# Kernel tuning notes

Hardware: AMD Instinct MI355X
Metric: run time of the kernel (lower is better)

The kernel has to match this reference:

```python
import jax, jax.numpy as jnp
import numpy as np

B, T, C = 4, 2048, 1024
H = 16
DH = C // H  # 64


def setup_inputs() -> dict:
    key = jax.random.key(0)
    ks = jax.random.split(key, 6)
    s = 1.0 / np.sqrt(C)
    x = jax.random.normal(ks[0], (B, T, C), dtype=jnp.float32)
    # per-head projection weights, stacked: (H, C, DH)
    Wq = jax.random.uniform(ks[1], (H, C, DH), dtype=jnp.float32, minval=-s, maxval=s)
    Wk = jax.random.uniform(ks[2], (H, C, DH), dtype=jnp.float32, minval=-s, maxval=s)
    Wv = jax.random.uniform(ks[3], (H, C, DH), dtype=jnp.float32, minval=-s, maxval=s)
    # output projection (torch Linear: y = x @ W.T + b); store as (C, C) for x @ Wo
    Wo = jax.random.uniform(ks[4], (C, C), dtype=jnp.float32, minval=-s, maxval=s)
    bo = jax.random.uniform(ks[5], (C,), dtype=jnp.float32, minval=-s, maxval=s)
    return {"x": x, "Wq": Wq, "Wk": Wk, "Wv": Wv, "Wo": Wo, "bo": bo}


def reference(x, Wq, Wk, Wv, Wo, bo):
    # x: (B,T,C) -> q,k,v: (B,H,T,DH)
    q = jnp.einsum('btc,hcd->bhtd', x, Wq)
    k = jnp.einsum('btc,hcd->bhtd', x, Wk)
    v = jnp.einsum('btc,hcd->bhtd', x, Wv)
    scale = DH ** -0.5
    scores = jnp.einsum('bhtd,bhsd->bhts', q, k) * scale  # (B,H,T,T)
    causal = jnp.tril(jnp.ones((T, T), dtype=bool))
    scores = jnp.where(causal, scores, -jnp.inf)
    wei = jax.nn.softmax(scores, axis=-1)
    out = jnp.einsum('bhts,bhsd->bhtd', wei, v)  # (B,H,T,DH)
    # concat heads: (B,T,H*DH) = (B,T,C)
    out = out.transpose(0, 2, 1, 3).reshape(B, T, C)
    return out @ Wo + bo
```

## Files before the change

### kernel.cpp

```cpp
#include <hip/hip_runtime.h>

#define T_SEQ 2048
#define C_DIM 1024
#define H_NUM 16
#define DHD   64
#define B_NUM 4
#define M_ROWS (B_NUM*T_SEQ)

typedef __bf16 bf16x8 __attribute__((ext_vector_type(8)));
typedef float  f32x4  __attribute__((ext_vector_type(4)));
typedef unsigned short ushort8 __attribute__((ext_vector_type(8)));
typedef unsigned short ushort4e __attribute__((ext_vector_type(4)));

__device__ __forceinline__ unsigned short f2b(float f){
  return __builtin_bit_cast(unsigned short, (__bf16)f);
}
__device__ __forceinline__ bf16x8 as_bf(ushort8 u){ return __builtin_bit_cast(bf16x8, u); }
__device__ __forceinline__ float exp2fast(float x){ return __builtin_amdgcn_exp2f(x); }

__device__ __forceinline__ void gload16(const void* g, void* l){
  __builtin_amdgcn_global_load_lds(
      (const __attribute__((address_space(1))) void*)g,
      (__attribute__((address_space(3))) void*)l, 16, 0, 0);
}

#define MF(a,b,c) __builtin_amdgcn_mfma_f32_16x16x32_bf16(a,b,c,0,0,0)

__global__ __launch_bounds__(256) void k_prep(const float* __restrict__ x,
                                              const float* __restrict__ wq,
                                              const float* __restrict__ wk,
                                              const float* __restrict__ wv,
                                              const float* __restrict__ wo,
                                              unsigned short* __restrict__ xb,
                                              unsigned short* __restrict__ wt,
                                              unsigned short* __restrict__ wot){
  const int bid = blockIdx.x;
  if (bid < 8192){
    int i = bid*256 + threadIdx.x;
    float4 f = ((const float4*)x)[i];
    ushort4e o;
    o[0]=f2b(f.x); o[1]=f2b(f.y); o[2]=f2b(f.z); o[3]=f2b(f.w);
    ((ushort4e*)xb)[i] = o;
  } else {
    int idx = (bid - 8192)*256 + threadIdx.x;
    if (idx < 3*C_DIM*C_DIM){
      int nall = idx >> 10; int c = idx & 1023;
      int m = nall >> 10;   int n = nall & 1023;
      int h = n >> 6, d = n & 63;
      const float* w = (m==0) ? wq : (m==1) ? wk : wv;
      float f = w[((size_t)h*C_DIM + c)*DHD + d];
      if (m == 0) f *= 0.125f * 1.4426950408889634f;
      wt[idx] = f2b(f);
    } else {
      int j = idx - 3*C_DIM*C_DIM;
      int n = j >> 10, c = j & 1023;
      wot[j] = f2b(wo[(size_t)c*C_DIM + n]);
    }
  }
}

__global__ __launch_bounds__(256) void k_gemm_qkv(const unsigned short* __restrict__ xb,
                                                  const unsigned short* __restrict__ wt,
                                                  unsigned short* __restrict__ qo,
                                                  unsigned short* __restrict__ ko,
                                                  unsigned short* __restrict__ vtr){
  __shared__ __align__(16) unsigned short smem[2][128*64];
  const int tid = threadIdx.x, lane = tid & 63, wid = tid >> 6;
  const int g = lane >> 4, tl = lane & 15;
  const int wr = wid >> 1, wc = wid & 1;
  const int id = blockIdx.x;
  const int xcd = id & 7, i = id >> 3;
  const int xm = xcd >> 1, xn = xcd & 1;
  const int mbase = (xm*16 + i/12) * 128, nbase = (xn*12 + i%12) * 128;
  f32x4 acc[4][4] = {};
  for (int kk = 0; kk < C_DIM; kk += 64){
    __syncthreads();
    #pragma unroll
    for (int i2 = 0; i2 < 4; i2++){
      const int brow = (wid*4 + i2)*8;
      const int row  = brow + (lane >> 3);
      const int jj   = (lane & 7) ^ (row & 7);
      gload16(&xb[(size_t)(mbase+row)*C_DIM + kk + jj*8], &smem[0][brow*64]);
      gload16(&wt[(size_t)(nbase+row)*C_DIM + kk + jj*8], &smem[1][brow*64]);
    }
    __syncthreads();
    bf16x8 aF[4][2], bF[4][2];
    #pragma unroll
    for (int mb = 0; mb < 4; mb++){
      const int row = wr*64 + mb*16 + tl; const int s7 = row & 7;
      aF[mb][0] = as_bf(*(const ushort8*)&smem[0][row*64 + ((g     ^ s7)*8)]);
      aF[mb][1] = as_bf(*(const ushort8*)&smem[0][row*64 + (((4+g) ^ s7)*8)]);
    }
    #pragma unroll
    for (int nb = 0; nb < 4; nb++){
      const int row = wc*64 + nb*16 + tl; const int s7 = row & 7;
      bF[nb][0] = as_bf(*(const ushort8*)&smem[1][row*64 + ((g     ^ s7)*8)]);
      bF[nb][1] = as_bf(*(const ushort8*)&smem[1][row*64 + (((4+g) ^ s7)*8)]);
    }
    #pragma unroll
    for (int mb = 0; mb < 4; mb++)
      #pragma unroll
      for (int nb = 0; nb < 4; nb++){
        acc[mb][nb] = MF(aF[mb][0], bF[nb][0], acc[mb][nb]);
        acc[mb][nb] = MF(aF[mb][1], bF[nb][1], acc[mb][nb]);
      }
  }
  const int sel = nbase >> 10;
  if (sel < 2){
    unsigned short* dst0 = (sel == 0) ? qo : ko;
    #pragma unroll
    for (int mb = 0; mb < 4; mb++){
      #pragma unroll
      for (int nb = 0; nb < 4; nb++){
        #pragma unroll
        for (int r = 0; r < 4; r++){
          int gr = mbase + wr*64 + mb*16 + g*4 + r;
          int gc = nbase + wc*64 + nb*16 + tl;
          int b = gr >> 11, t = gr & 2047;
          int nw = gc & 1023;
          int h = nw >> 6, d = nw & 63;
          dst0[(((size_t)(b*H_NUM + h))*T_SEQ + t)*DHD + d] = f2b(acc[mb][nb][r]);
        }
      }
    }
  } else {
    __syncthreads();
    unsigned short* tr = &smem[0][0];
    #pragma unroll
    for (int mb = 0; mb < 4; mb++){
      #pragma unroll
      for (int nb = 0; nb < 4; nb++){
        const int n = wc*64 + nb*16 + tl;
        const int m0 = wr*64 + mb*16 + g*4;
        ushort4e pk;
        #pragma unroll
        for (int r = 0; r < 4; r++) pk[r] = f2b(acc[mb][nb][r]);
        *(ushort4e*)&tr[n*128 + (m0 ^ ((n & 15) << 3))] = pk;
      }
    }
    __syncthreads();
    const int hbase = (nbase - 2048) >> 6;
    const int b = mbase >> 11, tloc = mbase & 2047;
    const int n = tid >> 1, half = tid & 1;
    unsigned short* vdst = vtr + (((size_t)(b*H_NUM + hbase + (n >> 6)))*DHD + (n & 63))*T_SEQ
                           + tloc + half*64;
    const int nx = (n & 15) << 3;
    #pragma unroll
    for (int c8 = 0; c8 < 8; c8++){
      const int t0 = half*64 + (c8 >> 2)*32 + (c8 & 3)*4;
      ushort4e lo = *(const ushort4e*)&tr[n*128 + ((t0     ) ^ nx)];
      ushort4e hi = *(const ushort4e*)&tr[n*128 + ((t0 + 16) ^ nx)];
      ushort8 u;
      #pragma unroll
      for (int e = 0; e < 4; e++){ u[e] = lo[e]; u[4+e] = hi[e]; }
      *(ushort8*)&vdst[c8*8] = u;
    }
  }
}

__global__ __launch_bounds__(512) void k_flash(const unsigned short* __restrict__ q,
                                               const unsigned short* __restrict__ k,
                                               const unsigned short* __restrict__ vtg,
                                               unsigned short* __restrict__ o){
  __shared__ __align__(16) unsigned short kbufs[2][128*64];
  __shared__ __align__(16) unsigned short vbufs[2][64*128];
  const int tid = threadIdx.x, lane = tid & 63, w = tid >> 6;
  const int g = lane >> 4, tl = lane & 15;
  const int id = blockIdx.x;
  const int swz = (id & 7)*32 + (id >> 3);
  const int bh = swz >> 2, bx = swz & 3;
  const int b = bh >> 4, h = bh & 15;
  const unsigned short* qb = q   + (size_t)bh * T_SEQ * DHD;
  const unsigned short* kb = k   + (size_t)bh * T_SEQ * DHD;
  const unsigned short* vb = vtg + (size_t)bh * (size_t)DHD * T_SEQ;
  const int lrow = lane >> 3, lj = lane & 7;
  const int s7 = tl & 7;
  const int vre = lane >> 4;
  const int vh  = (lane >> 3) & 1;
  const int vcc = lane & 7;

  for (int pass = 0; pass < 2; ++pass){
    const int qt = pass ? (7 - bx) : bx;
    const int tbase = qt * 256;
    const int trow0 = tbase + w * 32;
    const int tmax = trow0 + 31;
    bf16x8 qF[2][2];
    #pragma unroll
    for (int tf = 0; tf < 2; tf++)
      #pragma unroll
      for (int ks = 0; ks < 2; ks++)
        qF[tf][ks] = as_bf(*(const ushort8*)&qb[(size_t)(trow0 + tf*16 + tl)*DHD + ks*32 + g*8]);
    f32x4 acc[2][4] = {};
    float mreg[2] = {-1e30f, -1e30f}, lreg[2] = {0.f, 0.f};
    const int nkt = 2*qt + 2;
    #pragma unroll
    for (int i = 0; i < 2; i++){
      const int krow = i*64 + w*8 + lrow;
      const int kjj  = lj ^ (krow & 7);
      gload16(&kb[(size_t)krow*DHD + kjj*8], &kbufs[0][(i*64 + w*8)*64]);
      const int vrow = i*32 + w*4 + vre;
      const int vjj  = vcc ^ (vrow & 7);
      gload16(&vb[(size_t)vrow*T_SEQ + vh*64 + vjj*8], &vbufs[0][(i*32 + w*4)*128]);
    }
    __syncthreads();
    for (int kti = 0; kti < nkt; ++kti){
      const int cur = kti & 1;
      const int kbase = kti * 128;
      if (kti + 1 < nkt){
        const int kb2 = kbase + 128;
        #pragma unroll
        for (int i = 0; i < 2; i++){
          const int krow = i*64 + w*8 + lrow;
          const int kjj  = lj ^ (krow & 7);
          gload16(&kb[(size_t)(kb2+krow)*DHD + kjj*8], &kbufs[cur^1][(i*64 + w*8)*64]);
          const int vrow = i*32 + w*4 + vre;
          const int vjj  = vcc ^ (vrow & 7);
          gload16(&vb[(size_t)vrow*T_SEQ + kb2 + vh*64 + vjj*8], &vbufs[cur^1][(i*32 + w*4)*128]);
        }
      }
      if (kbase <= tmax){
        const unsigned short* kcur = kbufs[cur];
        const unsigned short* vcur = vbufs[cur];
        f32x4 st[2][8] = {};
        __builtin_amdgcn_s_setprio(1);
        #pragma unroll
        for (int sf = 0; sf < 8; sf++){
          const int row = sf*16 + tl;
          const int r7 = row & 7;
          bf16x8 kf0 = as_bf(*(const ushort8*)&kcur[row*64 + ((g     ^ r7)*8)]);
          bf16x8 kf1 = as_bf(*(const ushort8*)&kcur[row*64 + (((4+g) ^ r7)*8)]);
          #pragma unroll
          for (int tf = 0; tf < 2; tf++){
            st[tf][sf] = MF(kf0, qF[tf][0], st[tf][sf]);
            st[tf][sf] = MF(kf1, qF[tf][1], st[tf][sf]);
          }
        }
        __builtin_amdgcn_s_setprio(0);
        if (kbase + 127 > trow0){
          #pragma unroll
          for (int tf = 0; tf < 2; tf++){
            int tg = trow0 + tf*16 + tl;
            #pragma unroll
            for (int sf = 0; sf < 8; sf++)
              #pragma unroll
              for (int r = 0; r < 4; r++)
                if (kbase + sf*16 + g*4 + r > tg) st[tf][sf][r] = -1e30f;
          }
        }
        bf16x8 pa[2][4];
        #pragma unroll
        for (int tf = 0; tf < 2; tf++){
          float mloc = -1e30f;
          #pragma unroll
          for (int sf = 0; sf < 8; sf++)
            #pragma unroll
            for (int r = 0; r < 4; r++) mloc = fmaxf(mloc, st[tf][sf][r]);
          if (__any(mloc > mreg[tf] + 8.f)){
            float mrow = fmaxf(mloc, __shfl_xor(mloc, 16));
            mrow = fmaxf(mrow, __shfl_xor(mrow, 32));
            float mnew = fmaxf(mreg[tf], mrow);
            float alpha = exp2fast(mreg[tf] - mnew);
            mreg[tf] = mnew;
            lreg[tf] *= alpha;
            #pragma unroll
            for (int df = 0; df < 4; df++)
              #pragma unroll
              for (int r = 0; r < 4; r++) acc[tf][df][r] *= alpha;
          }
          float sum = 0.f;
          #pragma unroll
          for (int q4 = 0; q4 < 4; q4++){
            ushort8 u;
            #pragma unroll
            for (int r = 0; r < 4; r++){
              float p0 = exp2fast(st[tf][2*q4  ][r] - mreg[tf]);
              float p1 = exp2fast(st[tf][2*q4+1][r] - mreg[tf]);
              sum += p0 + p1;
              u[r]   = f2b(p0);
              u[4+r] = f2b(p1);
            }
            pa[tf][q4] = as_bf(u);
          }
          lreg[tf] += sum;
        }
        __builtin_amdgcn_s_setprio(1);
        #pragma unroll
        for (int df = 0; df < 4; df++){
          const int row = df*16 + tl;
          bf16x8 vfr[4];
          #pragma unroll
          for (int q4 = 0; q4 < 4; q4++)
            vfr[q4] = as_bf(*(const ushort8*)&vcur[row*128 + (q4 >> 1)*64 + (((4*(q4 & 1) + g) ^ s7)*8)]);
          #pragma unroll
          for (int tf = 0; tf < 2; tf++)
            #pragma unroll
            for (int q4 = 0; q4 < 4; q4++)
              acc[tf][df] = MF(vfr[q4], pa[tf][q4], acc[tf][df]);
        }
        __builtin_amdgcn_s_setprio(0);
      }
      __syncthreads();
    }
    #pragma unroll
    for (int tf = 0; tf < 2; tf++){
      float l = lreg[tf];
      l += __shfl_xor(l, 16);
      l += __shfl_xor(l, 32);
      float inv = 1.f / l;
      int tg = trow0 + tf*16 + tl;
      #pragma unroll
      for (int df = 0; df < 4; df++){
        ushort4e ov;
        #pragma unroll
        for (int r = 0; r < 4; r++) ov[r] = f2b(acc[tf][df][r] * inv);
        *(ushort4e*)&o[((size_t)(b*T_SEQ + tg))*C_DIM + h*DHD + df*16 + g*4] = ov;
      }
    }
  }
}

__global__ __launch_bounds__(256) void k_gemm_proj(const unsigned short* __restrict__ ab,
                                                   const unsigned short* __restrict__ wot,
                                                   const float* __restrict__ bo,
                                                   float* __restrict__ out){
  __shared__ __align__(16) unsigned short a_lds[128*64];
  __shared__ __align__(16) unsigned short b_lds[128*64];
  const int tid = threadIdx.x, lane = tid & 63, wid = tid >> 6;
  const int g = lane >> 4, tl = lane & 15;
  const int wr = wid >> 1, wc = wid & 1;
  const int id = blockIdx.x;
  const int swz = (id & 7)*64 + (id >> 3);
  const int mbase = (swz >> 3) * 128, nbase = (swz & 7) * 128;
  f32x4 acc[4][4] = {};
  for (int kk = 0; kk < C_DIM; kk += 64){
    __syncthreads();
    #pragma unroll
    for (int i = 0; i < 4; i++){
      const int brow = (wid*4 + i)*8;
      const int row  = brow + (lane >> 3);
      const int jj   = (lane & 7) ^ (row & 7);
      gload16(&ab[(size_t)(mbase+row)*C_DIM + kk + jj*8],  &a_lds[brow*64]);
      gload16(&wot[(size_t)(nbase+row)*C_DIM + kk + jj*8], &b_lds[brow*64]);
    }
    __syncthreads();
    bf16x8 aF[4][2], bF[4][2];
    #pragma unroll
    for (int mb = 0; mb < 4; mb++){
      const int row = wr*64 + mb*16 + tl; const int s7 = row & 7;
      aF[mb][0] = as_bf(*(const ushort8*)&a_lds[row*64 + ((g     ^ s7)*8)]);
      aF[mb][1] = as_bf(*(const ushort8*)&a_lds[row*64 + (((4+g) ^ s7)*8)]);
    }
    #pragma unroll
    for (int nb = 0; nb < 4; nb++){
      const int row = wc*64 + nb*16 + tl; const int s7 = row & 7;
      bF[nb][0] = as_bf(*(const ushort8*)&b_lds[row*64 + ((g     ^ s7)*8)]);
      bF[nb][1] = as_bf(*(const ushort8*)&b_lds[row*64 + (((4+g) ^ s7)*8)]);
    }
    #pragma unroll
    for (int mb = 0; mb < 4; mb++)
      #pragma unroll
      for (int nb = 0; nb < 4; nb++){
        acc[mb][nb] = MF(aF[mb][0], bF[nb][0], acc[mb][nb]);
        acc[mb][nb] = MF(aF[mb][1], bF[nb][1], acc[mb][nb]);
      }
  }
  #pragma unroll
  for (int mb = 0; mb < 4; mb++){
    #pragma unroll
    for (int nb = 0; nb < 4; nb++){
      #pragma unroll
      for (int r = 0; r < 4; r++){
        int gr = mbase + wr*64 + mb*16 + g*4 + r;
        int gc = nbase + wc*64 + nb*16 + tl;
        out[(size_t)gr*C_DIM + gc] = acc[mb][nb][r] + bo[gc];
      }
    }
  }
}

extern "C" void kernel_launch(void* const* d_in, const int* in_sizes, int n_in,
                              void* d_out, int out_size, void* d_ws, size_t ws_size,
                              hipStream_t stream){
  const float* x  = (const float*)d_in[0];
  const float* Wq = (const float*)d_in[1];
  const float* Wk = (const float*)d_in[2];
  const float* Wv = (const float*)d_in[3];
  const float* Wo = (const float*)d_in[4];
  const float* bo = (const float*)d_in[5];
  float* out = (float*)d_out;

  char* p = (char*)d_ws;
  unsigned short* xb  = (unsigned short*)p; p += (size_t)M_ROWS*C_DIM*2;
  unsigned short* wt  = (unsigned short*)p; p += (size_t)3*C_DIM*C_DIM*2;
  unsigned short* wot = (unsigned short*)p; p += (size_t)C_DIM*C_DIM*2;
  unsigned short* Qb  = (unsigned short*)p; p += (size_t)M_ROWS*C_DIM*2;
  unsigned short* Kb  = (unsigned short*)p; p += (size_t)M_ROWS*C_DIM*2;
  unsigned short* Vtr = (unsigned short*)p; p += (size_t)M_ROWS*C_DIM*2;
  unsigned short* attn = xb;

  hipLaunchKernelGGL(k_prep, dim3(8192 + 16384), dim3(256), 0, stream,
                     x, Wq, Wk, Wv, Wo, xb, wt, wot);
  hipLaunchKernelGGL(k_gemm_qkv, dim3(1536), dim3(256), 0, stream,
                     xb, wt, Qb, Kb, Vtr);
  hipLaunchKernelGGL(k_flash, dim3(256), dim3(512), 0, stream,
                     Qb, Kb, Vtr, attn);
  hipLaunchKernelGGL(k_gemm_proj, dim3(512), dim3(256), 0, stream,
                     attn, wot, bo, out);
}
```

Measured before the change: 174.1 us.

## Split KV tile across wave halves in flash attention with LDS merge

```diff
diff --git a/kernel.cpp b/kernel.cpp
--- a/kernel.cpp
+++ b/kernel.cpp
@@ -164,7 +164,9 @@
                                                unsigned short* __restrict__ o){
   __shared__ __align__(16) unsigned short kbufs[2][128*64];
   __shared__ __align__(16) unsigned short vbufs[2][64*128];
+  __shared__ __align__(16) float cbuf[4][64][72];
   const int tid = threadIdx.x, lane = tid & 63, w = tid >> 6;
+  const int whalf = w >> 2, wq = w & 3;
   const int g = lane >> 4, tl = lane & 15;
   const int id = blockIdx.x;
   const int swz = (id & 7)*32 + (id >> 3);
@@ -182,16 +184,18 @@
   for (int pass = 0; pass < 2; ++pass){
     const int qt = pass ? (7 - bx) : bx;
     const int tbase = qt * 256;
-    const int trow0 = tbase + w * 32;
-    const int tmax = trow0 + 31;
-    bf16x8 qF[2][2];
-    #pragma unroll
-    for (int tf = 0; tf < 2; tf++)
+    const int trow0 = tbase + wq * 64;
+    const int tmax = trow0 + 63;
+    bf16x8 qF[4][2];
+    #pragma unroll
+    for (int tf = 0; tf < 4; tf++)
       #pragma unroll
       for (int ks = 0; ks < 2; ks++)
         qF[tf][ks] = as_bf(*(const ushort8*)&qb[(size_t)(trow0 + tf*16 + tl)*DHD + ks*32 + g*8]);
-    f32x4 acc[2][4] = {};
-    float mreg[2] = {-1e30f, -1e30f}, lreg[2] = {0.f, 0.f};
+    f32x4 acc[4][4] = {};
+    float mreg[4], lreg[4];
+    #pragma unroll
+    for (int tf = 0; tf < 4; tf++){ mreg[tf] = -1e30f; lreg[tf] = 0.f; }
     const int nkt = 2*qt + 2;
     #pragma unroll
     for (int i = 0; i < 2; i++){
@@ -218,41 +222,42 @@
           gload16(&vb[(size_t)vrow*T_SEQ + kb2 + vh*64 + vjj*8], &vbufs[cur^1][(i*32 + w*4)*128]);
         }
       }
-      if (kbase <= tmax){
+      const int smin = kbase + whalf*64;
+      if (smin <= tmax){
         const unsigned short* kcur = kbufs[cur];
         const unsigned short* vcur = vbufs[cur];
-        f32x4 st[2][8] = {};
+        f32x4 st[4][4] = {};
         __builtin_amdgcn_s_setprio(1);
         #pragma unroll
-        for (int sf = 0; sf < 8; sf++){
-          const int row = sf*16 + tl;
+        for (int sf = 0; sf < 4; sf++){
+          const int row = whalf*64 + sf*16 + tl;
           const int r7 = row & 7;
           bf16x8 kf0 = as_bf(*(const ushort8*)&kcur[row*64 + ((g     ^ r7)*8)]);
           bf16x8 kf1 = as_bf(*(const ushort8*)&kcur[row*64 + (((4+g) ^ r7)*8)]);
           #pragma unroll
-          for (int tf = 0; tf < 2; tf++){
+          for (int tf = 0; tf < 4; tf++){
             st[tf][sf] = MF(kf0, qF[tf][0], st[tf][sf]);
             st[tf][sf] = MF(kf1, qF[tf][1], st[tf][sf]);
           }
         }
         __builtin_amdgcn_s_setprio(0);
-        if (kbase + 127 > trow0){
-          #pragma unroll
-          for (int tf = 0; tf < 2; tf++){
+        if (smin + 63 > trow0){
+          #pragma unroll
+          for (int tf = 0; tf < 4; tf++){
             int tg = trow0 + tf*16 + tl;
             #pragma unroll
-            for (int sf = 0; sf < 8; sf++)
+            for (int sf = 0; sf < 4; sf++)
               #pragma unroll
               for (int r = 0; r < 4; r++)
-                if (kbase + sf*16 + g*4 + r > tg) st[tf][sf][r] = -1e30f;
+                if (smin + sf*16 + g*4 + r > tg) st[tf][sf][r] = -1e30f;
           }
         }
-        bf16x8 pa[2][4];
-        #pragma unroll
-        for (int tf = 0; tf < 2; tf++){
+        bf16x8 pa[4][2];
+        #pragma unroll
+        for (int tf = 0; tf < 4; tf++){
           float mloc = -1e30f;
           #pragma unroll
-          for (int sf = 0; sf < 8; sf++)
+          for (int sf = 0; sf < 4; sf++)
             #pragma unroll
             for (int r = 0; r < 4; r++) mloc = fmaxf(mloc, st[tf][sf][r]);
           if (__any(mloc > mreg[tf] + 8.f)){
@@ -269,17 +274,17 @@
           }
           float sum = 0.f;
           #pragma unroll
-          for (int q4 = 0; q4 < 4; q4++){
-            ushort8 u;
+          for (int ks2 = 0; ks2 < 2; ks2++){
+            ushort8 uu;
             #pragma unroll
             for (int r = 0; r < 4; r++){
-              float p0 = exp2fast(st[tf][2*q4  ][r] - mreg[tf]);
-              float p1 = exp2fast(st[tf][2*q4+1][r] - mreg[tf]);
+              float p0 = exp2fast(st[tf][2*ks2  ][r] - mreg[tf]);
+              float p1 = exp2fast(st[tf][2*ks2+1][r] - mreg[tf]);
               sum += p0 + p1;
-              u[r]   = f2b(p0);
-              u[4+r] = f2b(p1);
+              uu[r]   = f2b(p0);
+              uu[4+r] = f2b(p1);
             }
-            pa[tf][q4] = as_bf(u);
+            pa[tf][ks2] = as_bf(uu);
           }
           lreg[tf] += sum;
         }
@@ -287,35 +292,63 @@
         #pragma unroll
         for (int df = 0; df < 4; df++){
           const int row = df*16 + tl;
-          bf16x8 vfr[4];
-          #pragma unroll
-          for (int q4 = 0; q4 < 4; q4++)
-            vfr[q4] = as_bf(*(const ushort8*)&vcur[row*128 + (q4 >> 1)*64 + (((4*(q4 & 1) + g) ^ s7)*8)]);
-          #pragma unroll
-          for (int tf = 0; tf < 2; tf++)
+          bf16x8 vfr[2];
+          #pragma unroll
+          for (int ks2 = 0; ks2 < 2; ks2++){
+            const int q4 = whalf*2 + ks2;
+            vfr[ks2] = as_bf(*(const ushort8*)&vcur[row*128 + (q4 >> 1)*64 + (((4*(q4 & 1) + g) ^ s7)*8)]);
+          }
+          #pragma unroll
+          for (int tf = 0; tf < 4; tf++)
             #pragma unroll
-            for (int q4 = 0; q4 < 4; q4++)
-              acc[tf][df] = MF(vfr[q4], pa[tf][q4], acc[tf][df]);
+            for (int ks2 = 0; ks2 < 2; ks2++)
+              acc[tf][df] = MF(vfr[ks2], pa[tf][ks2], acc[tf][df]);
         }
         __builtin_amdgcn_s_setprio(0);
       }
       __syncthreads();
     }
-    #pragma unroll
-    for (int tf = 0; tf < 2; tf++){
+    float lfin[4];
+    #pragma unroll
+    for (int tf = 0; tf < 4; tf++){
       float l = lreg[tf];
       l += __shfl_xor(l, 16);
       l += __shfl_xor(l, 32);
-      float inv = 1.f / l;
-      int tg = trow0 + tf*16 + tl;
-      #pragma unroll
-      for (int df = 0; df < 4; df++){
-        ushort4e ov;
-        #pragma unroll
-        for (int r = 0; r < 4; r++) ov[r] = f2b(acc[tf][df][r] * inv);
-        *(ushort4e*)&o[((size_t)(b*T_SEQ + tg))*C_DIM + h*DHD + df*16 + g*4] = ov;
-      }
-    }
+      lfin[tf] = l;
+    }
+    if (whalf == 1){
+      #pragma unroll
+      for (int tf = 0; tf < 4; tf++){
+        #pragma unroll
+        for (int df = 0; df < 4; df++)
+          *(f32x4*)&cbuf[wq][lane][(tf*4 + df)*4] = acc[tf][df];
+        cbuf[wq][lane][64 + tf] = mreg[tf];
+        cbuf[wq][lane][68 + tf] = lfin[tf];
+      }
+    }
+    __syncthreads();
+    if (whalf == 0){
+      #pragma unroll
+      for (int tf = 0; tf < 4; tf++){
+        float m1 = cbuf[wq][lane][64 + tf];
+        float l1 = cbuf[wq][lane][68 + tf];
+        float m = fmaxf(mreg[tf], m1);
+        float a0 = exp2fast(mreg[tf] - m);
+        float a1 = exp2fast(m1 - m);
+        float inv = 1.f / (a0*lfin[tf] + a1*l1);
+        int tg = trow0 + tf*16 + tl;
+        #pragma unroll
+        for (int df = 0; df < 4; df++){
+          f32x4 o1 = *(const f32x4*)&cbuf[wq][lane][(tf*4 + df)*4];
+          ushort4e ov;
+          #pragma unroll
+          for (int r = 0; r < 4; r++)
+            ov[r] = f2b((a0*acc[tf][df][r] + a1*o1[r]) * inv);
+          *(ushort4e*)&o[((size_t)(b*T_SEQ + tg))*C_DIM + h*DHD + df*16 + g*4] = ov;
+        }
+      }
+    }
+    __syncthreads();
   }
 }
 
```

New measurement: 177.0 us. No clear change (+1.7%).
